# Performance work log

Hardware: AMD Instinct MI355X
Metric: run time of the kernel (lower is better)

The kernel has to match this reference:

```python
import jax, jax.numpy as jnp
import numpy as np

CUTOFF = 5.0
MAX_NBR = 32      # max_num_neighbors
LOOP = True
B, M = 128, 1024  # molecules, atoms per molecule (batch is uniform: batch[i] = i // M)
BOX = 26.0        # box side chosen so ~30 atoms fall within CUTOFF


def setup_inputs() -> dict:
    key = jax.random.key(0)
    pos = jax.random.uniform(key, (B * M, 3), dtype=jnp.float32) * BOX
    batch = jnp.repeat(jnp.arange(B, dtype=jnp.int32), M)
    return {"pos": pos, "batch": batch}


def reference(pos, batch):
    # radius_graph with per-graph (molecule) candidate search. Equal-size
    # molecules (batch = arange // M) let us use a dense [B, M, M] candidate
    # matrix per molecule; truncation keeps the K nearest within cutoff
    # (PyG keeps an arbitrary K within cutoff; nearest-K is the deterministic
    # variant). Output has fixed shape [2, B*M*K] padded with self-loops.
    posb = pos.reshape(B, M, 3)
    sq = jnp.sum(posb * posb, axis=-1)                       # [B, M]
    dot = jnp.einsum('bmd,bnd->bmn', posb, posb)             # [B, M, M]
    d2 = jnp.maximum(sq[:, :, None] + sq[:, None, :] - 2.0 * dot, 0.0)
    within = d2 <= CUTOFF * CUTOFF
    if not LOOP:
        within = within & ~jnp.eye(M, dtype=bool)[None]
    neg = jnp.where(within, -d2, -jnp.inf)
    vals, idx = jax.lax.top_k(neg, MAX_NBR)                  # [B, M, K]
    valid = jnp.isfinite(vals)
    center = jnp.arange(M, dtype=idx.dtype)[None, :, None]   # [1, M, 1]
    idx_eff = jnp.where(valid, idx, center)                  # pad invalid -> self

    b_ix = jnp.arange(B)[:, None, None]
    nbr = posb[b_ix, idx_eff]                                # [B, M, K, 3]
    edge_vec = nbr - posb[:, :, None, :]                     # pos[src] - pos[dst]

    is_self = idx_eff == center
    wmask = valid & ~is_self                                 # self-loops get weight 0
    d2sel = jnp.sum(edge_vec * edge_vec, axis=-1)
    edge_weight = jnp.where(wmask, jnp.sqrt(jnp.where(wmask, d2sel, 1.0)), 0.0)

    offs = (jnp.arange(B, dtype=idx.dtype) * M)[:, None, None]
    src = (offs + idx_eff).reshape(-1)                       # neighbor (edge_index[0])
    dst = jnp.broadcast_to(offs + center, (B, M, MAX_NBR)).reshape(-1)
    edge_index = jnp.stack([src, dst])                       # [2, B*M*K]
    return edge_index, edge_weight.reshape(-1), edge_vec.reshape(-1, 3)
```

## Files before the change

### kernel.cpp

```cpp
#include <hip/hip_runtime.h>

#define NB 128
#define NM 1024
#define NK 32
#define NS 16
#define CUT2 25.0f
#define CUT2_BITS 0x41C80000u
#define KEYMASK   0xFFFFFC00u

typedef unsigned int   u32;
typedef unsigned short u16;
typedef float vf4 __attribute__((ext_vector_type(4)));

__global__ __launch_bounds__(256) void pack_atoms(const float* __restrict__ pos,
                                                  float4* __restrict__ scanb,
                                                  float4* __restrict__ rawb, int dual)
{
  int i = blockIdx.x * 256 + threadIdx.x;
  float x = pos[3*i+0], y = pos[3*i+1], z = pos[3*i+2];
  float sq = x*x + y*y + z*z;
  rawb[i] = make_float4(x, y, z, sq);
  if (dual) scanb[i] = make_float4(-2.f*x, -2.f*y, -2.f*z, sq);
}

__device__ __forceinline__ void ce_asc(u32 &a, u32 &b) {
  u32 mn = a < b ? a : b;
  u32 mx = a < b ? b : a;
  a = mn; b = mx;
}

template <int N, int K, int D>
__device__ __forceinline__ void bitonic_pass(u32* r) {
#pragma unroll
  for (int i = 0; i < N; ++i)
    if ((i & D) == 0) {
      if ((i & K) == 0) ce_asc(r[i], r[i | D]);
      else              ce_asc(r[i | D], r[i]);
    }
}

template <bool NEG2>
__global__ __launch_bounds__(256, 4) void radius_knn(const float4* __restrict__ scanb,
                                                     const float4* __restrict__ rawb,
                                                     float* __restrict__ out)
{
  __shared__ float xs[NM], ys[NM], zs[NM], sqs[NM];
  __shared__ u32 lmem[4096];
  u16* lists = (u16*)lmem;

  const int tid  = threadIdx.x;
  const int lane = tid & 127;
  const int half = tid >> 7;
  const int molb = blockIdx.x & 127;
  const int q8   = blockIdx.x >> 7;
  const int c    = molb * NM + q8 * 128 + lane;
  const int mloc = c & (NM - 1);

  const float4* st = rawb + (size_t)molb * NM;
  for (int t = tid; t < NM; t += 256) {
    float4 a = st[t];
    xs[t] = a.x; ys[t] = a.y; zs[t] = a.z; sqs[t] = a.w;
  }
  __syncthreads();

  const float mex = xs[mloc], mey = ys[mloc], mez = zs[mloc], mew = sqs[mloc];

  const float4* mp = scanb + ((size_t)(c >> 10) << 10);
  const int jbase = half * 512;
  int cnt = 0;
  float4 ta[8], tb[8];
#pragma unroll
  for (int u = 0; u < 8; ++u) ta[u] = mp[jbase + u];

  auto body = [&](const float4* t, int j0) {
#pragma unroll
    for (int u = 0; u < 8; ++u) {
      float d2;
      if (NEG2) {
        d2 = __builtin_fmaf(mex, t[u].x,
             __builtin_fmaf(mey, t[u].y,
             __builtin_fmaf(mez, t[u].z, mew + t[u].w)));
      } else {
        float dot = (mex*t[u].x + mey*t[u].y) + mez*t[u].z;
        d2 = __builtin_fmaf(-2.f, dot, mew + t[u].w);
      }
      int slot = cnt < NS ? cnt : (NS - 1);
      lists[slot * 256 + tid] = (u16)(j0 + u);
      cnt += (d2 <= CUT2) ? 1 : 0;
    }
  };

  for (int g = 0; g < 64; g += 2) {
    const int j1 = jbase + (((g + 1) & 63) << 3);
#pragma unroll
    for (int u = 0; u < 8; ++u) tb[u] = mp[j1 + u];
    body(ta, jbase + (g << 3));
    const int j2 = jbase + (((g + 2) & 63) << 3);
#pragma unroll
    for (int u = 0; u < 8; ++u) ta[u] = mp[j2 + u];
    body(tb, jbase + ((g + 1) << 3));
  }
  if (cnt > NS) cnt = NS;

  const u32 PADK = 0x7F800000u | (u32)mloc;
  u32 r[NK];
#pragma unroll
  for (int k = 0; k < NS; ++k) {
    u32 key = PADK;
    if (k < cnt) {
      int j = lists[k * 256 + tid];
      float dot = (mex*xs[j] + mey*ys[j]) + mez*zs[j];
      float d2  = fmaxf((mew + sqs[j]) - 2.f*dot, 0.f);
      key = (__float_as_uint(d2) & KEYMASK) | (u32)j;
    }
    r[k] = key;
  }
  bitonic_pass<16, 2, 1>(r);
  bitonic_pass<16, 4, 2>(r); bitonic_pass<16, 4, 1>(r);
  bitonic_pass<16, 8, 4>(r); bitonic_pass<16, 8, 2>(r); bitonic_pass<16, 8, 1>(r);
  bitonic_pass<16,16, 8>(r); bitonic_pass<16,16, 4>(r); bitonic_pass<16,16, 2>(r); bitonic_pass<16,16, 1>(r);

  __syncthreads();
  {
    u32* myp = lmem + half * 2048 + lane * 16;
#pragma unroll
    for (int k = 0; k < NS; ++k) myp[(k + lane) & 15] = r[k];
  }
  __syncthreads();
  {
    u32* op = lmem + (1 - half) * 2048 + lane * 16;
#pragma unroll
    for (int i = 0; i < NS; ++i) r[16 + i] = op[((15 - i) + lane) & 15];
  }
  bitonic_pass<32,32,16>(r); bitonic_pass<32,32, 8>(r); bitonic_pass<32,32, 4>(r);
  bitonic_pass<32,32, 2>(r); bitonic_pass<32,32, 1>(r);

  const long long E = (long long)NB * NM * NK;
  const float base = (float)((c >> 10) * NM);

  if (!half) {
    vf4* ps = (vf4*)(out       + (size_t)c * NK);
    vf4* pd = (vf4*)(out +   E + (size_t)c * NK);
    vf4* pw = (vf4*)(out + 2*E + (size_t)c * NK);
    const float fc = (float)c;
    const vf4 dstv = {fc, fc, fc, fc};
#pragma unroll
    for (int q = 0; q < 8; ++q) {
      float sv[4], wv[4];
#pragma unroll
      for (int u = 0; u < 4; ++u) {
        u32 key = r[4*q + u];
        int idx = (int)(key & 1023u);
        bool valid = (key & KEYMASK) <= CUT2_BITS;
        float vx = xs[idx] - mex;
        float vy = ys[idx] - mey;
        float vz = zs[idx] - mez;
        bool wm  = valid && (idx != mloc);
        float d2s = vx*vx + vy*vy + vz*vz;
        wv[u] = wm ? sqrtf(d2s) : 0.0f;
        sv[u] = base + (float)idx;
      }
      ps[q] = (vf4){sv[0], sv[1], sv[2], sv[3]};
      pd[q] = dstv;
      pw[q] = (vf4){wv[0], wv[1], wv[2], wv[3]};
    }
  } else {
    vf4* pv = (vf4*)(out + 3*E + (size_t)c * NK * 3);
#pragma unroll
    for (int q = 0; q < 8; ++q) {
      float vv[12];
#pragma unroll
      for (int u = 0; u < 4; ++u) {
        int idx = (int)(r[4*q + u] & 1023u);
        vv[3*u+0] = xs[idx] - mex;
        vv[3*u+1] = ys[idx] - mey;
        vv[3*u+2] = zs[idx] - mez;
      }
      pv[3*q+0] = (vf4){vv[0], vv[1], vv[2],  vv[3]};
      pv[3*q+1] = (vf4){vv[4], vv[5], vv[6],  vv[7]};
      pv[3*q+2] = (vf4){vv[8], vv[9], vv[10], vv[11]};
    }
  }
}

extern "C" void kernel_launch(void* const* d_in, const int* in_sizes, int n_in,
                              void* d_out, int out_size, void* d_ws, size_t ws_size,
                              hipStream_t stream) {
  const float* pos = (const float*)d_in[0];
  float* out = (float*)d_out;
  const size_t one = (size_t)NB * NM * sizeof(float4);

  if (ws_size >= 2 * one) {
    float4* scanb = (float4*)d_ws;
    float4* rawb  = (float4*)((char*)d_ws + one);
    hipLaunchKernelGGL(pack_atoms, dim3((NB*NM)/256), dim3(256), 0, stream,
                       pos, scanb, rawb, 1);
    hipLaunchKernelGGL((radius_knn<true>), dim3(2*(NB*NM)/256), dim3(256), 0, stream,
                       scanb, rawb, out);
  } else {
    float4* rawb = (float4*)d_ws;
    hipLaunchKernelGGL(pack_atoms, dim3((NB*NM)/256), dim3(256), 0, stream,
                       pos, rawb, rawb, 0);
    hipLaunchKernelGGL((radius_knn<false>), dim3(2*(NB*NM)/256), dim3(256), 0, stream,
                       rawb, rawb, out);
  }
}
```

Measured before the change: 192.0 us.

## Replace brute-force all-pairs scan with per-molecule cell-list binning

Atoms of each molecule are binned into a 5x5x5 grid of cells sized to the cutoff and written out sorted by cell, keeping their original index. The search kernel then scans only the 27 neighbouring cells instead of all 1024 atoms, split between the two thread halves by cell parity. This removes most of the distance evaluations and global loads from the candidate scan. In exchange it adds a binning kernel with a serial 125-thread scatter loop and per-thread divergent cell loops. It also hardcodes the box size into INVCELL and assumes coordinates are non-negative, and the output order for ties and truncation can differ from the previous atom-index order.

```diff
diff --git a/kernel.cpp b/kernel.cpp
--- a/kernel.cpp
+++ b/kernel.cpp
@@ -7,20 +7,52 @@
 #define CUT2 25.0f
 #define CUT2_BITS 0x41C80000u
 #define KEYMASK   0xFFFFFC00u
+#define INVCELL   0.19230769f
 
 typedef unsigned int   u32;
 typedef unsigned short u16;
 typedef float vf4 __attribute__((ext_vector_type(4)));
 
-__global__ __launch_bounds__(256) void pack_atoms(const float* __restrict__ pos,
-                                                  float4* __restrict__ scanb,
-                                                  float4* __restrict__ rawb, int dual)
+__device__ __forceinline__ int cell_of(float x, float y, float z) {
+  int cx = (int)(x * INVCELL); cx = cx > 4 ? 4 : cx;
+  int cy = (int)(y * INVCELL); cy = cy > 4 ? 4 : cy;
+  int cz = (int)(z * INVCELL); cz = cz > 4 ? 4 : cz;
+  return (cx * 5 + cy) * 5 + cz;
+}
+
+__global__ __launch_bounds__(256) void bin_mol(const float* __restrict__ pos,
+                                               float4* __restrict__ reorder)
 {
-  int i = blockIdx.x * 256 + threadIdx.x;
-  float x = pos[3*i+0], y = pos[3*i+1], z = pos[3*i+2];
-  float sq = x*x + y*y + z*z;
-  rawb[i] = make_float4(x, y, z, sq);
-  if (dual) scanb[i] = make_float4(-2.f*x, -2.f*y, -2.f*z, sq);
+  __shared__ float raw[3 * NM];
+  __shared__ u16   cellid[NM];
+  __shared__ int   counts[125];
+  __shared__ int   start[125];
+  const int tid = threadIdx.x, mol = blockIdx.x;
+  const float* mp = pos + (size_t)mol * NM * 3;
+  for (int t = tid; t < 3 * NM; t += 256) raw[t] = mp[t];
+  if (tid < 125) counts[tid] = 0;
+  __syncthreads();
+  for (int i = tid; i < NM; i += 256) {
+    int cid = cell_of(raw[3*i], raw[3*i+1], raw[3*i+2]);
+    cellid[i] = (u16)cid;
+    atomicAdd(&counts[cid], 1);
+  }
+  __syncthreads();
+  if (tid == 0) {
+    int s = 0;
+    for (int c2 = 0; c2 < 125; ++c2) { start[c2] = s; s += counts[c2]; }
+  }
+  __syncthreads();
+  if (tid < 125) {
+    int cur = start[tid];
+    float4* dst = reorder + ((size_t)mol << 10);
+    for (int i = 0; i < NM; ++i) {
+      if (cellid[i] == tid) {
+        dst[cur] = make_float4(raw[3*i], raw[3*i+1], raw[3*i+2], __int_as_float(i));
+        ++cur;
+      }
+    }
+  }
 }
 
 __device__ __forceinline__ void ce_asc(u32 &a, u32 &b) {
@@ -39,13 +71,12 @@
     }
 }
 
-template <bool NEG2>
-__global__ __launch_bounds__(256, 4) void radius_knn(const float4* __restrict__ scanb,
-                                                     const float4* __restrict__ rawb,
-                                                     float* __restrict__ out)
+__global__ __launch_bounds__(256, 4) void radius_cell(const float4* __restrict__ reorder,
+                                                      float* __restrict__ out)
 {
-  __shared__ float xs[NM], ys[NM], zs[NM], sqs[NM];
-  __shared__ u32 lmem[4096];
+  __shared__ float4 atoms[NM];
+  __shared__ int    cstart[126];
+  __shared__ u32    lmem[4096];
   u16* lists = (u16*)lmem;
 
   const int tid  = threadIdx.x;
@@ -53,64 +84,62 @@
   const int half = tid >> 7;
   const int molb = blockIdx.x & 127;
   const int q8   = blockIdx.x >> 7;
-  const int c    = molb * NM + q8 * 128 + lane;
-  const int mloc = c & (NM - 1);
-
-  const float4* st = rawb + (size_t)molb * NM;
+
+  const float4* mp = reorder + ((size_t)molb << 10);
+  for (int t = tid; t < NM; t += 256) atoms[t] = mp[t];
+  __syncthreads();
+
   for (int t = tid; t < NM; t += 256) {
-    float4 a = st[t];
-    xs[t] = a.x; ys[t] = a.y; zs[t] = a.z; sqs[t] = a.w;
-  }
-  __syncthreads();
-
-  const float mex = xs[mloc], mey = ys[mloc], mez = zs[mloc], mew = sqs[mloc];
-
-  const float4* mp = scanb + ((size_t)(c >> 10) << 10);
-  const int jbase = half * 512;
-  int cnt = 0;
-  float4 ta[8], tb[8];
-#pragma unroll
-  for (int u = 0; u < 8; ++u) ta[u] = mp[jbase + u];
-
-  auto body = [&](const float4* t, int j0) {
-#pragma unroll
-    for (int u = 0; u < 8; ++u) {
-      float d2;
-      if (NEG2) {
-        d2 = __builtin_fmaf(mex, t[u].x,
-             __builtin_fmaf(mey, t[u].y,
-             __builtin_fmaf(mez, t[u].z, mew + t[u].w)));
-      } else {
-        float dot = (mex*t[u].x + mey*t[u].y) + mez*t[u].z;
-        d2 = __builtin_fmaf(-2.f, dot, mew + t[u].w);
-      }
-      int slot = cnt < NS ? cnt : (NS - 1);
-      lists[slot * 256 + tid] = (u16)(j0 + u);
-      cnt += (d2 <= CUT2) ? 1 : 0;
-    }
-  };
-
-  for (int g = 0; g < 64; g += 2) {
-    const int j1 = jbase + (((g + 1) & 63) << 3);
-#pragma unroll
-    for (int u = 0; u < 8; ++u) tb[u] = mp[j1 + u];
-    body(ta, jbase + (g << 3));
-    const int j2 = jbase + (((g + 2) & 63) << 3);
-#pragma unroll
-    for (int u = 0; u < 8; ++u) ta[u] = mp[j2 + u];
-    body(tb, jbase + ((g + 1) << 3));
-  }
+    float4 a1 = atoms[t];
+    int c1 = cell_of(a1.x, a1.y, a1.z);
+    int c0 = -1;
+    if (t > 0) { float4 a0 = atoms[t-1]; c0 = cell_of(a0.x, a0.y, a0.z); }
+    for (int c2 = c0 + 1; c2 <= c1; ++c2) cstart[c2] = t;
+    if (t == NM - 1) for (int c2 = c1 + 1; c2 <= 125; ++c2) cstart[c2] = NM;
+  }
+  __syncthreads();
+
+  const int spos = q8 * 128 + lane;
+  const float4 me = atoms[spos];
+  const int mloc = __float_as_int(me.w);
+  const int c    = (molb << 10) + mloc;
+  const float mex = me.x, mey = me.y, mez = me.z;
+
+  int cx = (int)(mex * INVCELL); cx = cx > 4 ? 4 : cx;
+  int cy = (int)(mey * INVCELL); cy = cy > 4 ? 4 : cy;
+  int cz = (int)(mez * INVCELL); cz = cz > 4 ? 4 : cz;
+  const int x0 = cx > 0 ? cx-1 : 0, x1 = cx < 4 ? cx+1 : 4;
+  const int y0 = cy > 0 ? cy-1 : 0, y1 = cy < 4 ? cy+1 : 4;
+  const int z0 = cz > 0 ? cz-1 : 0, z1 = cz < 4 ? cz+1 : 4;
+
+  int cnt = 0, par = 0;
+  for (int xx = x0; xx <= x1; ++xx)
+    for (int yy = y0; yy <= y1; ++yy)
+      for (int zz = z0; zz <= z1; ++zz) {
+        if (((par++) & 1) != half) continue;
+        int cid = (xx * 5 + yy) * 5 + zz;
+        int s = cstart[cid], e = cstart[cid + 1];
+        for (int k = s; k < e; ++k) {
+          float4 a = atoms[k];
+          float dx = a.x - mex, dy = a.y - mey, dz = a.z - mez;
+          float d2 = __builtin_fmaf(dx, dx, __builtin_fmaf(dy, dy, dz * dz));
+          int slot = cnt < NS ? cnt : (NS - 1);
+          lists[slot * 256 + tid] = (u16)k;
+          cnt += (d2 <= CUT2) ? 1 : 0;
+        }
+      }
   if (cnt > NS) cnt = NS;
 
-  const u32 PADK = 0x7F800000u | (u32)mloc;
+  const u32 PADK = 0x7F800000u | (u32)spos;
   u32 r[NK];
 #pragma unroll
   for (int k = 0; k < NS; ++k) {
     u32 key = PADK;
     if (k < cnt) {
       int j = lists[k * 256 + tid];
-      float dot = (mex*xs[j] + mey*ys[j]) + mez*zs[j];
-      float d2  = fmaxf((mew + sqs[j]) - 2.f*dot, 0.f);
+      float4 a = atoms[j];
+      float dx = a.x - mex, dy = a.y - mey, dz = a.z - mez;
+      float d2 = __builtin_fmaf(dx, dx, __builtin_fmaf(dy, dy, dz * dz));
       key = (__float_as_uint(d2) & KEYMASK) | (u32)j;
     }
     r[k] = key;
@@ -136,7 +165,7 @@
   bitonic_pass<32,32, 2>(r); bitonic_pass<32,32, 1>(r);
 
   const long long E = (long long)NB * NM * NK;
-  const float base = (float)((c >> 10) * NM);
+  const float base = (float)(molb << 10);
 
   if (!half) {
     vf4* ps = (vf4*)(out       + (size_t)c * NK);
@@ -150,15 +179,14 @@
 #pragma unroll
       for (int u = 0; u < 4; ++u) {
         u32 key = r[4*q + u];
-        int idx = (int)(key & 1023u);
+        int sp  = (int)(key & 1023u);
+        float4 a = atoms[sp];
         bool valid = (key & KEYMASK) <= CUT2_BITS;
-        float vx = xs[idx] - mex;
-        float vy = ys[idx] - mey;
-        float vz = zs[idx] - mez;
-        bool wm  = valid && (idx != mloc);
+        float vx = a.x - mex, vy = a.y - mey, vz = a.z - mez;
+        bool wm  = valid && (sp != spos);
         float d2s = vx*vx + vy*vy + vz*vz;
         wv[u] = wm ? sqrtf(d2s) : 0.0f;
-        sv[u] = base + (float)idx;
+        sv[u] = base + (float)__float_as_int(a.w);
       }
       ps[q] = (vf4){sv[0], sv[1], sv[2], sv[3]};
       pd[q] = dstv;
@@ -171,10 +199,11 @@
       float vv[12];
 #pragma unroll
       for (int u = 0; u < 4; ++u) {
-        int idx = (int)(r[4*q + u] & 1023u);
-        vv[3*u+0] = xs[idx] - mex;
-        vv[3*u+1] = ys[idx] - mey;
-        vv[3*u+2] = zs[idx] - mez;
+        int sp = (int)(r[4*q + u] & 1023u);
+        float4 a = atoms[sp];
+        vv[3*u+0] = a.x - mex;
+        vv[3*u+1] = a.y - mey;
+        vv[3*u+2] = a.z - mez;
       }
       pv[3*q+0] = (vf4){vv[0], vv[1], vv[2],  vv[3]};
       pv[3*q+1] = (vf4){vv[4], vv[5], vv[6],  vv[7]};
@@ -188,20 +217,8 @@
                               hipStream_t stream) {
   const float* pos = (const float*)d_in[0];
   float* out = (float*)d_out;
-  const size_t one = (size_t)NB * NM * sizeof(float4);
-
-  if (ws_size >= 2 * one) {
-    float4* scanb = (float4*)d_ws;
-    float4* rawb  = (float4*)((char*)d_ws + one);
-    hipLaunchKernelGGL(pack_atoms, dim3((NB*NM)/256), dim3(256), 0, stream,
-                       pos, scanb, rawb, 1);
-    hipLaunchKernelGGL((radius_knn<true>), dim3(2*(NB*NM)/256), dim3(256), 0, stream,
-                       scanb, rawb, out);
-  } else {
-    float4* rawb = (float4*)d_ws;
-    hipLaunchKernelGGL(pack_atoms, dim3((NB*NM)/256), dim3(256), 0, stream,
-                       pos, rawb, rawb, 0);
-    hipLaunchKernelGGL((radius_knn<false>), dim3(2*(NB*NM)/256), dim3(256), 0, stream,
-                       rawb, rawb, out);
-  }
-}
+  float4* reorder = (float4*)d_ws;
+
+  hipLaunchKernelGGL(bin_mol,     dim3(NB),   dim3(256), 0, stream, pos, reorder);
+  hipLaunchKernelGGL(radius_cell, dim3(1024), dim3(256), 0, stream, reorder, out);
+}
```

After: 231.5 us. +20.6%, slower.
